# Kernel optimization log

Measured on AMD Instinct MI355X. Metric: run time of the kernel, lower is better.

## Reference

```python
import jax, jax.numpy as jnp
import numpy as np

STRIDES = (8.0, 16.0, 32.0)
ANCHORS = np.array([[[12,16],[19,36],[40,28]],
                    [[36,75],[76,55],[72,146]],
                    [[142,110],[192,243],[459,401]]], dtype=np.float32)  # [3 levels, 3 anchors, 2] in input pixels
INPUT_SIZE = 416.0
IGNORE_THRESHOLD = 0.5
EPS = 1e-7
MAX_BOXES = 64  # fixed cap on true boxes per image for jit-able ignore-mask
NC = 80


def _bce_logits(logits, targets):
    # numerically-stable binary cross entropy with logits, elementwise
    return jnp.maximum(logits, 0.0) - logits * targets + jnp.log1p(jnp.exp(-jnp.abs(logits)))


def _iou_xywh(b1, b2):
    # center-format boxes, broadcastable; returns IoU over last dim pair
    a1 = b1[..., 2] * b1[..., 3]
    a2 = b2[..., 2] * b2[..., 3]
    lt = jnp.maximum(b1[..., :2] - b1[..., 2:] * 0.5, b2[..., :2] - b2[..., 2:] * 0.5)
    rb = jnp.minimum(b1[..., :2] + b1[..., 2:] * 0.5, b2[..., :2] + b2[..., 2:] * 0.5)
    wh = jnp.maximum(rb - lt, 0.0)
    inter = wh[..., 0] * wh[..., 1]
    union = a1 + a2 - inter
    return inter / jnp.maximum(union, 1e-9)


def _level_loss(feature, label, idx):
    N, C, H, W = feature.shape
    f = feature.transpose(0, 2, 3, 1).reshape(N, H, W, 3, -1)
    raw_xy, raw_wh = f[..., 0:2], f[..., 2:4]
    raw_conf, raw_prob = f[..., 4:5], f[..., 5:]

    label_xywh = label[..., 0:4]
    label_conf = label[..., 4:5]
    label_prob = label[..., 5:]

    stride = STRIDES[idx]
    anchors = jnp.asarray(ANCHORS[idx])  # [3,2]

    gy, gx = jnp.meshgrid(jnp.arange(H, dtype=f.dtype), jnp.arange(W, dtype=f.dtype), indexing='ij')
    grid = jnp.stack([gx, gy], axis=-1)[:, :, None, :]  # [H,W,1,2]

    # decode predictions (GeneratePrediction)
    pred_xy = (jax.nn.sigmoid(raw_xy) + grid) * stride
    pred_wh = jnp.exp(raw_wh) * anchors
    pred_xywh = jnp.concatenate([pred_xy, pred_wh], axis=-1)  # [N,H,W,3,4]

    xy_offset = label_xywh[..., :2] / stride - grid
    wh_offset = label_conf * jnp.log(label_xywh[..., 2:4] / anchors + EPS)
    bbox_loss_scale = 2.0 - label_xywh[..., 2:3] * label_xywh[..., 3:4] / (INPUT_SIZE * INPUT_SIZE)

    # ignore mask: max IoU of each prediction against this image's true boxes
    conf_flat = label_conf[..., 0].reshape(N, -1)          # [N, H*W*3]
    boxes_flat = label_xywh.reshape(N, -1, 4)              # [N, H*W*3, 4]
    k = min(MAX_BOXES, conf_flat.shape[1])
    vals, idxs = jax.lax.top_k(conf_flat, k)               # positives first (conf is 0/1)
    true_boxes = jnp.take_along_axis(boxes_flat, idxs[..., None], axis=1)  # [N,k,4]
    valid = vals > 0.0                                     # [N,k]
    iou = _iou_xywh(pred_xywh[..., None, :], true_boxes[:, None, None, None, :, :])  # [N,H,W,3,k]
    iou = jnp.where(valid[:, None, None, None, :], iou, 0.0)
    max_iou = jnp.max(iou, axis=-1)                        # [N,H,W,3]; 0 when no valid boxes
    ignore_mask = (max_iou < IGNORE_THRESHOLD).astype(f.dtype)[..., None]

    xy_loss = label_conf * bbox_loss_scale * _bce_logits(raw_xy, xy_offset)
    wh_loss = label_conf * bbox_loss_scale * 0.5 * jnp.square(raw_wh - wh_offset)
    bce_conf = _bce_logits(raw_conf, label_conf)
    conf_loss = label_conf * bce_conf + (1.0 - label_conf) * ignore_mask * bce_conf
    prob_loss = label_conf * _bce_logits(raw_prob, label_prob)

    sum_axes = (1, 2, 3, 4)
    reg = jnp.mean(jnp.sum(xy_loss, axis=sum_axes)) + jnp.mean(jnp.sum(wh_loss, axis=sum_axes))
    conf = jnp.mean(jnp.sum(conf_loss, axis=sum_axes))
    prob = jnp.mean(jnp.sum(prob_loss, axis=sum_axes))
    return reg, conf, prob


def _make_label(key, N, H, W, p_pos):
    kc, kxy, kwh, kp = jax.random.split(key, 4)
    conf = (jax.random.uniform(kc, (N, H, W, 3, 1)) < p_pos).astype(jnp.float32)
    xy = jax.random.uniform(kxy, (N, H, W, 3, 2)) * INPUT_SIZE
    wh = jax.random.uniform(kwh, (N, H, W, 3, 2)) * 190.0 + 10.0  # strictly positive
    prob = (jax.random.uniform(kp, (N, H, W, 3, NC)) < 0.0125).astype(jnp.float32)
    return jnp.concatenate([xy, wh, conf, prob], axis=-1)


def setup_inputs() -> dict:
    key = jax.random.key(0)
    ks = jax.random.split(key, 6)
    N, C = 16, 3 * (5 + NC)
    sizes = [52, 26, 13]
    preds = [jax.random.normal(ks[i], (N, C, s, s), dtype=jnp.float32) for i, s in enumerate(sizes)]
    labels = [_make_label(ks[3 + i], N, s, s, 0.0008) for i, s in enumerate(sizes)]
    return {"pred0": preds[0], "pred1": preds[1], "pred2": preds[2],
            "label0": labels[0], "label1": labels[1], "label2": labels[2]}


def reference(pred0, pred1, pred2, label0, label1, label2):
    reg = conf = prob = 0.0
    for i, (f, l) in enumerate([(pred0, label0), (pred1, label1), (pred2, label2)]):
        r, c, p = _level_loss(f, l, i)
        reg, conf, prob = reg + r, conf + c, prob + p
    return (reg, conf, prob)
```

## Files before the change

kernel.cpp:

```cpp
#include <hip/hip_runtime.h>


#define NIMG 16
#define MAXB 64

#define C0 (16 * 3 * 52 * 52)
#define C1 (16 * 3 * 26 * 26)
#define C2 (16 * 3 * 13 * 13)
#define CTOT (C0 + C1 + C2)
#define NBLK ((CTOT + 255) / 256)

#define WS_COUNTS   0
#define WS_BOXES    256
#define WS_CELLIDS  49408
#define WS_PARTIAL  65536

__device__ __constant__ float d_anchors[3][3][2] = {
    {{12.f, 16.f}, {19.f, 36.f}, {40.f, 28.f}},
    {{36.f, 75.f}, {76.f, 55.f}, {72.f, 146.f}},
    {{142.f, 110.f}, {192.f, 243.f}, {459.f, 401.f}}};

__device__ __forceinline__ float bce_logits(float x, float t) {
    return fmaxf(x, 0.f) - x * t + log1pf(expf(-fabsf(x)));
}

__global__ void scan_labels(const float* __restrict__ l0,
                            const float* __restrict__ l1,
                            const float* __restrict__ l2,
                            int* __restrict__ counts,
                            float4* __restrict__ boxes,
                            int* __restrict__ cellids) {
    int rec = blockIdx.x * blockDim.x + threadIdx.x;
    if (rec >= CTOT) return;

    const float* lab;
    int level, cell, hw3;
    if (rec < C0)           { level = 0; cell = rec;           lab = l0; hw3 = 3 * 52 * 52; }
    else if (rec < C0 + C1) { level = 1; cell = rec - C0;      lab = l1; hw3 = 3 * 26 * 26; }
    else                    { level = 2; cell = rec - C0 - C1; lab = l2; hw3 = 3 * 13 * 13; }

    const float* lp = lab + (size_t)cell * 85;
    float c = lp[4];
    if (c > 0.f) {
        int n = cell / hw3;
        int p = atomicAdd(&counts[level * NIMG + n], 1);
        if (p < MAXB) {
            float4 b;
            b.x = lp[0]; b.y = lp[1]; b.z = lp[2]; b.w = lp[3];
            boxes[(level * NIMG + n) * MAXB + p] = b;
            cellids[(level * NIMG + n) * MAXB + p] = cell;
        }
    }
}

__global__ void loss_fused(const float* __restrict__ f0,
                           const float* __restrict__ f1,
                           const float* __restrict__ f2,
                           const float* __restrict__ l0,
                           const float* __restrict__ l1,
                           const float* __restrict__ l2,
                           const int* __restrict__ counts,
                           const float4* __restrict__ boxes,
                           const int* __restrict__ cellids,
                           float* __restrict__ partial) {
    int lane = threadIdx.x & 63;
    int wid = threadIdx.x >> 6;

    if (blockIdx.x < NBLK) {
        int gid = blockIdx.x * blockDim.x + threadIdx.x;
        float conf = 0.f;

        if (gid < CTOT) {
            const float* f;
            int level, cell, W, HW;
            float stride;
            if (gid < C0)           { level = 0; cell = gid;           f = f0; W = 52; HW = 52 * 52; stride = 8.f; }
            else if (gid < C0 + C1) { level = 1; cell = gid - C0;      f = f1; W = 26; HW = 26 * 26; stride = 16.f; }
            else                    { level = 2; cell = gid - C0 - C1; f = f2; W = 13; HW = 13 * 13; stride = 32.f; }

            int hw = cell % HW;
            int na = cell / HW;
            int a = na % 3;
            int n = na / 3;
            int w = hw % W;
            int h = hw / W;
            int cell_lab = (n * HW + hw) * 3 + a;

            const float* fp = f + (size_t)n * 255 * HW + (size_t)a * 85 * HW + hw;
            float rx = fp[0];
            float ry = fp[HW];
            float rw = fp[2 * HW];
            float rh = fp[3 * HW];
            float rc = fp[4 * HW];

            float aw = d_anchors[level][a][0];
            float ah = d_anchors[level][a][1];
            float px = (1.f / (1.f + expf(-rx)) + (float)w) * stride;
            float py = (1.f / (1.f + expf(-ry)) + (float)h) * stride;
            float pw = expf(rw) * aw;
            float ph = expf(rh) * ah;

            int m = counts[level * NIMG + n];
            if (m > MAXB) m = MAXB;
            int base = (level * NIMG + n) * MAXB;
            float parea = pw * ph;
            float pl = px - pw * 0.5f, pr = px + pw * 0.5f;
            float pt = py - ph * 0.5f, pb = py + ph * 0.5f;
            float maxiou = 0.f;
            bool ispos = false;
            for (int i = 0; i < m; ++i) {
                float4 b = boxes[base + i];
                if (cellids[base + i] == cell_lab) ispos = true;
                float tl = b.x - b.z * 0.5f, tr = b.x + b.z * 0.5f;
                float tt = b.y - b.w * 0.5f, tb = b.y + b.w * 0.5f;
                float iw = fmaxf(fminf(pr, tr) - fmaxf(pl, tl), 0.f);
                float ih = fmaxf(fminf(pb, tb) - fmaxf(pt, tt), 0.f);
                float inter = iw * ih;
                float uni = parea + b.z * b.w - inter;
                float iou = inter / fmaxf(uni, 1e-9f);
                maxiou = fmaxf(maxiou, iou);
            }
            if (ispos)              conf = bce_logits(rc, 1.f);
            else if (maxiou < 0.5f) conf = bce_logits(rc, 0.f);
        }

        for (int off = 32; off > 0; off >>= 1) conf += __shfl_down(conf, off);
        __shared__ float sc[4];
        if (lane == 0) sc[wid] = conf;
        __syncthreads();
        if (threadIdx.x == 0)
            partial[1 * 1024 + blockIdx.x] = sc[0] + sc[1] + sc[2] + sc[3];

    } else {
        int pb = blockIdx.x - NBLK;
        int level = pb / NIMG;
        int n = pb % NIMG;
        const float *f, *lab;
        int W, HW; float stride;
        if (level == 0)      { f = f0; lab = l0; W = 52; HW = 52 * 52; stride = 8.f; }
        else if (level == 1) { f = f1; lab = l1; W = 26; HW = 26 * 26; stride = 16.f; }
        else                 { f = f2; lab = l2; W = 13; HW = 13 * 13; stride = 32.f; }

        int m = counts[pb];
        if (m > MAXB) m = MAXB;
        int bbase = pb * MAXB;

        float reg_acc = 0.f, prob_acc = 0.f;
        for (int i = wid; i < m; i += 4) {
            int cell = cellids[bbase + i];
            float4 b = boxes[bbase + i];
            int a = cell % 3;
            int hw = (cell / 3) % HW;
            int w = hw % W;
            int h = hw / W;
            const float* fp = f + ((size_t)n * 255 + (size_t)a * 85) * HW + hw;
            const float* lp = lab + (size_t)cell * 85;

            int ch1 = (lane < 40) ? (5 + lane) : ((lane < 44) ? (lane - 40) : 0);
            float g1 = fp[(size_t)ch1 * HW];
            float g2 = fp[(size_t)((lane < 40) ? (45 + lane) : 0) * HW];
            float t1 = lp[(lane < 40) ? (5 + lane) : 0];
            float t2 = lp[(lane < 40) ? (45 + lane) : 0];

            float pp = (lane < 40) ? (bce_logits(g1, t1) + bce_logits(g2, t2)) : 0.f;
            for (int off = 32; off > 0; off >>= 1) pp += __shfl_down(pp, off);

            float rx = __shfl(g1, 40);
            float ry = __shfl(g1, 41);
            float rw = __shfl(g1, 42);
            float rh = __shfl(g1, 43);
            if (lane == 0) {
                prob_acc += pp;
                float aw = d_anchors[level][a][0];
                float ah = d_anchors[level][a][1];
                float ox = b.x / stride - (float)w;
                float oy = b.y / stride - (float)h;
                float ow = logf(b.z / aw + 1e-7f);
                float oh = logf(b.w / ah + 1e-7f);
                float scale = 2.f - b.z * b.w * (1.f / (416.f * 416.f));
                float dw = rw - ow, dh = rh - oh;
                reg_acc += scale * (bce_logits(rx, ox) + bce_logits(ry, oy))
                         + scale * 0.5f * (dw * dw + dh * dh);
            }
        }

        __shared__ float sp[2][4];
        if (lane == 0) { sp[0][wid] = reg_acc; sp[1][wid] = prob_acc; }
        __syncthreads();
        if (threadIdx.x == 0) {
            partial[0 * 1024 + pb] = sp[0][0] + sp[0][1] + sp[0][2] + sp[0][3];
            partial[2 * 1024 + pb] = sp[1][0] + sp[1][1] + sp[1][2] + sp[1][3];
        }
    }
}

__global__ void finalize(const float* __restrict__ partial,
                         float* __restrict__ out) {
    float a0 = 0.f, a1 = 0.f, a2 = 0.f;
    for (int i = threadIdx.x; i < NBLK; i += 256) {
        a1 += partial[1 * 1024 + i];
        if (i < 48) {
            a0 += partial[0 * 1024 + i];
            a2 += partial[2 * 1024 + i];
        }
    }
    for (int off = 32; off > 0; off >>= 1) {
        a0 += __shfl_down(a0, off);
        a1 += __shfl_down(a1, off);
        a2 += __shfl_down(a2, off);
    }
    __shared__ float s[3][4];
    int lane = threadIdx.x & 63;
    int wid = threadIdx.x >> 6;
    if (lane == 0) { s[0][wid] = a0; s[1][wid] = a1; s[2][wid] = a2; }
    __syncthreads();
    if (threadIdx.x == 0) {
        out[0] = (s[0][0] + s[0][1] + s[0][2] + s[0][3]) * (1.f / 16.f);
        out[1] = (s[1][0] + s[1][1] + s[1][2] + s[1][3]) * (1.f / 16.f);
        out[2] = (s[2][0] + s[2][1] + s[2][2] + s[2][3]) * (1.f / 16.f);
    }
}

extern "C" void kernel_launch(void* const* d_in, const int* in_sizes, int n_in,
                              void* d_out, int out_size, void* d_ws, size_t ws_size,
                              hipStream_t stream) {
    const float* f0 = (const float*)d_in[0];
    const float* f1 = (const float*)d_in[1];
    const float* f2 = (const float*)d_in[2];
    const float* l0 = (const float*)d_in[3];
    const float* l1 = (const float*)d_in[4];
    const float* l2 = (const float*)d_in[5];
    float* out = (float*)d_out;

    int*    counts  = (int*)((char*)d_ws + WS_COUNTS);
    float4* boxes   = (float4*)((char*)d_ws + WS_BOXES);
    int*    cellids = (int*)((char*)d_ws + WS_CELLIDS);
    float*  partial = (float*)((char*)d_ws + WS_PARTIAL);

    hipMemsetAsync(d_ws, 0, 256, stream);

    scan_labels<<<NBLK, 256, 0, stream>>>(l0, l1, l2, counts, boxes, cellids);
    loss_fused<<<NBLK + 48, 256, 0, stream>>>(f0, f1, f2, l0, l1, l2,
                                              counts, boxes, cellids, partial);
    finalize<<<1, 256, 0, stream>>>(partial, out);
}
```

Baseline: 134.3 us.

## Fuse scan, loss and finalize into one kernel with grid barrier

Merges the three launches into a single persistent kernel. A software grid barrier, built from an atomic counter and spin-sleep, separates the label scan from the loss phase. The prediction loads for the confidence path are issued before the barrier so they overlap the wait, and the last block to finish does the final reduction. This removes two kernel launches and their gaps, but it relies on all of the roughly 700 blocks being co-resident to avoid deadlock, and it adds spin contention on the barrier counter.

```diff
diff --git a/kernel.cpp b/kernel.cpp
--- a/kernel.cpp
+++ b/kernel.cpp
@@ -9,8 +9,10 @@
 #define C2 (16 * 3 * 13 * 13)
 #define CTOT (C0 + C1 + C2)
 #define NBLK ((CTOT + 255) / 256)
+#define NALL (NBLK + 48)
 
 #define WS_COUNTS   0
+#define WS_SYNC     192
 #define WS_BOXES    256
 #define WS_CELLIDS  49408
 #define WS_PARTIAL  65536
@@ -24,60 +26,77 @@
     return fmaxf(x, 0.f) - x * t + log1pf(expf(-fabsf(x)));
 }
 
-__global__ void scan_labels(const float* __restrict__ l0,
-                            const float* __restrict__ l1,
-                            const float* __restrict__ l2,
-                            int* __restrict__ counts,
-                            float4* __restrict__ boxes,
-                            int* __restrict__ cellids) {
-    int rec = blockIdx.x * blockDim.x + threadIdx.x;
-    if (rec >= CTOT) return;
-
-    const float* lab;
-    int level, cell, hw3;
-    if (rec < C0)           { level = 0; cell = rec;           lab = l0; hw3 = 3 * 52 * 52; }
-    else if (rec < C0 + C1) { level = 1; cell = rec - C0;      lab = l1; hw3 = 3 * 26 * 26; }
-    else                    { level = 2; cell = rec - C0 - C1; lab = l2; hw3 = 3 * 13 * 13; }
-
-    const float* lp = lab + (size_t)cell * 85;
-    float c = lp[4];
-    if (c > 0.f) {
-        int n = cell / hw3;
-        int p = atomicAdd(&counts[level * NIMG + n], 1);
-        if (p < MAXB) {
-            float4 b;
-            b.x = lp[0]; b.y = lp[1]; b.z = lp[2]; b.w = lp[3];
-            boxes[(level * NIMG + n) * MAXB + p] = b;
-            cellids[(level * NIMG + n) * MAXB + p] = cell;
-        }
-    }
-}
-
-__global__ void loss_fused(const float* __restrict__ f0,
-                           const float* __restrict__ f1,
-                           const float* __restrict__ f2,
-                           const float* __restrict__ l0,
-                           const float* __restrict__ l1,
-                           const float* __restrict__ l2,
-                           const int* __restrict__ counts,
-                           const float4* __restrict__ boxes,
-                           const int* __restrict__ cellids,
-                           float* __restrict__ partial) {
-    int lane = threadIdx.x & 63;
-    int wid = threadIdx.x >> 6;
-
-    if (blockIdx.x < NBLK) {
-        int gid = blockIdx.x * blockDim.x + threadIdx.x;
+__global__ __launch_bounds__(256) void yolo_all(
+        const float* __restrict__ f0,
+        const float* __restrict__ f1,
+        const float* __restrict__ f2,
+        const float* __restrict__ l0,
+        const float* __restrict__ l1,
+        const float* __restrict__ l2,
+        int* __restrict__ counts,
+        int* __restrict__ sync,
+        float4* __restrict__ boxes,
+        int* __restrict__ cellids,
+        float* __restrict__ partial,
+        float* __restrict__ out) {
+    const int lane = threadIdx.x & 63;
+    const int wid  = threadIdx.x >> 6;
+    const int tid  = blockIdx.x * blockDim.x + threadIdx.x;
+
+    if (tid < CTOT) {
+        const float* lab;
+        int level, cell, hw3;
+        if (tid < C0)           { level = 0; cell = tid;           lab = l0; hw3 = 3 * 52 * 52; }
+        else if (tid < C0 + C1) { level = 1; cell = tid - C0;      lab = l1; hw3 = 3 * 26 * 26; }
+        else                    { level = 2; cell = tid - C0 - C1; lab = l2; hw3 = 3 * 13 * 13; }
+        const float* lp = lab + (size_t)cell * 85;
+        float c = lp[4];
+        if (c > 0.f) {
+            int n = cell / hw3;
+            int p = atomicAdd(&counts[level * NIMG + n], 1);
+            if (p < MAXB) {
+                float4 b;
+                b.x = lp[0]; b.y = lp[1]; b.z = lp[2]; b.w = lp[3];
+                boxes[(level * NIMG + n) * MAXB + p] = b;
+                cellids[(level * NIMG + n) * MAXB + p] = cell;
+            }
+        }
+    }
+
+    const bool is_conf = (blockIdx.x < NBLK);
+    float rx = 0.f, ry = 0.f, rw = 0.f, rh = 0.f, rc = 0.f;
+    int level = 0, cell = 0, W = 52, HW = 52 * 52;
+    float stride = 8.f;
+    const float* fcur = f0;
+    if (is_conf && tid < CTOT) {
+        if (tid < C0)           { level = 0; cell = tid;           fcur = f0; W = 52; HW = 52 * 52; stride = 8.f; }
+        else if (tid < C0 + C1) { level = 1; cell = tid - C0;      fcur = f1; W = 26; HW = 26 * 26; stride = 16.f; }
+        else                    { level = 2; cell = tid - C0 - C1; fcur = f2; W = 13; HW = 13 * 13; stride = 32.f; }
+        int hw = cell % HW;
+        int na = cell / HW;
+        int a = na % 3;
+        int n = na / 3;
+        const float* fp = fcur + (size_t)n * 255 * HW + (size_t)a * 85 * HW + hw;
+        rx = fp[0];
+        ry = fp[HW];
+        rw = fp[2 * HW];
+        rh = fp[3 * HW];
+        rc = fp[4 * HW];
+    }
+
+    __syncthreads();
+    if (threadIdx.x == 0) {
+        __threadfence();
+        atomicAdd(&sync[0], 1);
+        while (atomicAdd(&sync[0], 0) < NALL)
+            __builtin_amdgcn_s_sleep(2);
+        __threadfence();
+    }
+    __syncthreads();
+
+    if (is_conf) {
         float conf = 0.f;
-
-        if (gid < CTOT) {
-            const float* f;
-            int level, cell, W, HW;
-            float stride;
-            if (gid < C0)           { level = 0; cell = gid;           f = f0; W = 52; HW = 52 * 52; stride = 8.f; }
-            else if (gid < C0 + C1) { level = 1; cell = gid - C0;      f = f1; W = 26; HW = 26 * 26; stride = 16.f; }
-            else                    { level = 2; cell = gid - C0 - C1; f = f2; W = 13; HW = 13 * 13; stride = 32.f; }
-
+        if (tid < CTOT) {
             int hw = cell % HW;
             int na = cell / HW;
             int a = na % 3;
@@ -85,13 +104,6 @@
             int w = hw % W;
             int h = hw / W;
             int cell_lab = (n * HW + hw) * 3 + a;
-
-            const float* fp = f + (size_t)n * 255 * HW + (size_t)a * 85 * HW + hw;
-            float rx = fp[0];
-            float ry = fp[HW];
-            float rw = fp[2 * HW];
-            float rh = fp[3 * HW];
-            float rc = fp[4 * HW];
 
             float aw = d_anchors[level][a][0];
             float ah = d_anchors[level][a][1];
@@ -123,23 +135,21 @@
             if (ispos)              conf = bce_logits(rc, 1.f);
             else if (maxiou < 0.5f) conf = bce_logits(rc, 0.f);
         }
-
         for (int off = 32; off > 0; off >>= 1) conf += __shfl_down(conf, off);
         __shared__ float sc[4];
         if (lane == 0) sc[wid] = conf;
         __syncthreads();
         if (threadIdx.x == 0)
             partial[1 * 1024 + blockIdx.x] = sc[0] + sc[1] + sc[2] + sc[3];
-
     } else {
         int pb = blockIdx.x - NBLK;
-        int level = pb / NIMG;
+        int lv = pb / NIMG;
         int n = pb % NIMG;
         const float *f, *lab;
-        int W, HW; float stride;
-        if (level == 0)      { f = f0; lab = l0; W = 52; HW = 52 * 52; stride = 8.f; }
-        else if (level == 1) { f = f1; lab = l1; W = 26; HW = 26 * 26; stride = 16.f; }
-        else                 { f = f2; lab = l2; W = 13; HW = 13 * 13; stride = 32.f; }
+        int Wp, HWp; float strp;
+        if (lv == 0)      { f = f0; lab = l0; Wp = 52; HWp = 52 * 52; strp = 8.f; }
+        else if (lv == 1) { f = f1; lab = l1; Wp = 26; HWp = 26 * 26; strp = 16.f; }
+        else              { f = f2; lab = l2; Wp = 13; HWp = 13 * 13; strp = 32.f; }
 
         int m = counts[pb];
         if (m > MAXB) m = MAXB;
@@ -147,43 +157,42 @@
 
         float reg_acc = 0.f, prob_acc = 0.f;
         for (int i = wid; i < m; i += 4) {
-            int cell = cellids[bbase + i];
+            int pcell = cellids[bbase + i];
             float4 b = boxes[bbase + i];
-            int a = cell % 3;
-            int hw = (cell / 3) % HW;
-            int w = hw % W;
-            int h = hw / W;
-            const float* fp = f + ((size_t)n * 255 + (size_t)a * 85) * HW + hw;
-            const float* lp = lab + (size_t)cell * 85;
+            int a = pcell % 3;
+            int hw = (pcell / 3) % HWp;
+            int w = hw % Wp;
+            int h = hw / Wp;
+            const float* fp = f + ((size_t)n * 255 + (size_t)a * 85) * HWp + hw;
+            const float* lp = lab + (size_t)pcell * 85;
 
             int ch1 = (lane < 40) ? (5 + lane) : ((lane < 44) ? (lane - 40) : 0);
-            float g1 = fp[(size_t)ch1 * HW];
-            float g2 = fp[(size_t)((lane < 40) ? (45 + lane) : 0) * HW];
+            float g1 = fp[(size_t)ch1 * HWp];
+            float g2 = fp[(size_t)((lane < 40) ? (45 + lane) : 0) * HWp];
             float t1 = lp[(lane < 40) ? (5 + lane) : 0];
             float t2 = lp[(lane < 40) ? (45 + lane) : 0];
 
             float pp = (lane < 40) ? (bce_logits(g1, t1) + bce_logits(g2, t2)) : 0.f;
             for (int off = 32; off > 0; off >>= 1) pp += __shfl_down(pp, off);
 
-            float rx = __shfl(g1, 40);
-            float ry = __shfl(g1, 41);
-            float rw = __shfl(g1, 42);
-            float rh = __shfl(g1, 43);
+            float prx = __shfl(g1, 40);
+            float pry = __shfl(g1, 41);
+            float prw = __shfl(g1, 42);
+            float prh = __shfl(g1, 43);
             if (lane == 0) {
                 prob_acc += pp;
-                float aw = d_anchors[level][a][0];
-                float ah = d_anchors[level][a][1];
-                float ox = b.x / stride - (float)w;
-                float oy = b.y / stride - (float)h;
+                float aw = d_anchors[lv][a][0];
+                float ah = d_anchors[lv][a][1];
+                float ox = b.x / strp - (float)w;
+                float oy = b.y / strp - (float)h;
                 float ow = logf(b.z / aw + 1e-7f);
                 float oh = logf(b.w / ah + 1e-7f);
                 float scale = 2.f - b.z * b.w * (1.f / (416.f * 416.f));
-                float dw = rw - ow, dh = rh - oh;
-                reg_acc += scale * (bce_logits(rx, ox) + bce_logits(ry, oy))
+                float dw = prw - ow, dh = prh - oh;
+                reg_acc += scale * (bce_logits(prx, ox) + bce_logits(pry, oy))
                          + scale * 0.5f * (dw * dw + dh * dh);
             }
         }
-
         __shared__ float sp[2][4];
         if (lane == 0) { sp[0][wid] = reg_acc; sp[1][wid] = prob_acc; }
         __syncthreads();
@@ -192,32 +201,38 @@
             partial[2 * 1024 + pb] = sp[1][0] + sp[1][1] + sp[1][2] + sp[1][3];
         }
     }
-}
-
-__global__ void finalize(const float* __restrict__ partial,
-                         float* __restrict__ out) {
-    float a0 = 0.f, a1 = 0.f, a2 = 0.f;
-    for (int i = threadIdx.x; i < NBLK; i += 256) {
-        a1 += partial[1 * 1024 + i];
-        if (i < 48) {
-            a0 += partial[0 * 1024 + i];
-            a2 += partial[2 * 1024 + i];
-        }
-    }
-    for (int off = 32; off > 0; off >>= 1) {
-        a0 += __shfl_down(a0, off);
-        a1 += __shfl_down(a1, off);
-        a2 += __shfl_down(a2, off);
-    }
-    __shared__ float s[3][4];
-    int lane = threadIdx.x & 63;
-    int wid = threadIdx.x >> 6;
-    if (lane == 0) { s[0][wid] = a0; s[1][wid] = a1; s[2][wid] = a2; }
+
+    __shared__ int amlast;
     __syncthreads();
     if (threadIdx.x == 0) {
-        out[0] = (s[0][0] + s[0][1] + s[0][2] + s[0][3]) * (1.f / 16.f);
-        out[1] = (s[1][0] + s[1][1] + s[1][2] + s[1][3]) * (1.f / 16.f);
-        out[2] = (s[2][0] + s[2][1] + s[2][2] + s[2][3]) * (1.f / 16.f);
+        __threadfence();
+        int d = atomicAdd(&sync[1], 1);
+        amlast = (d == NALL - 1) ? 1 : 0;
+    }
+    __syncthreads();
+    if (amlast) {
+        __threadfence();
+        float a0 = 0.f, a1 = 0.f, a2 = 0.f;
+        for (int i = threadIdx.x; i < NBLK; i += 256) {
+            a1 += partial[1 * 1024 + i];
+            if (i < 48) {
+                a0 += partial[0 * 1024 + i];
+                a2 += partial[2 * 1024 + i];
+            }
+        }
+        for (int off = 32; off > 0; off >>= 1) {
+            a0 += __shfl_down(a0, off);
+            a1 += __shfl_down(a1, off);
+            a2 += __shfl_down(a2, off);
+        }
+        __shared__ float s[3][4];
+        if (lane == 0) { s[0][wid] = a0; s[1][wid] = a1; s[2][wid] = a2; }
+        __syncthreads();
+        if (threadIdx.x == 0) {
+            out[0] = (s[0][0] + s[0][1] + s[0][2] + s[0][3]) * (1.f / 16.f);
+            out[1] = (s[1][0] + s[1][1] + s[1][2] + s[1][3]) * (1.f / 16.f);
+            out[2] = (s[2][0] + s[2][1] + s[2][2] + s[2][3]) * (1.f / 16.f);
+        }
     }
 }
 
@@ -233,14 +248,14 @@
     float* out = (float*)d_out;
 
     int*    counts  = (int*)((char*)d_ws + WS_COUNTS);
+    int*    syncp   = (int*)((char*)d_ws + WS_SYNC);
     float4* boxes   = (float4*)((char*)d_ws + WS_BOXES);
     int*    cellids = (int*)((char*)d_ws + WS_CELLIDS);
     float*  partial = (float*)((char*)d_ws + WS_PARTIAL);
 
     hipMemsetAsync(d_ws, 0, 256, stream);
 
-    scan_labels<<<NBLK, 256, 0, stream>>>(l0, l1, l2, counts, boxes, cellids);
-    loss_fused<<<NBLK + 48, 256, 0, stream>>>(f0, f1, f2, l0, l1, l2,
-                                              counts, boxes, cellids, partial);
-    finalize<<<1, 256, 0, stream>>>(partial, out);
+    yolo_all<<<NALL, 256, 0, stream>>>(f0, f1, f2, l0, l1, l2,
+                                       counts, syncp, boxes, cellids,
+                                       partial, out);
 }
```

After: 225.0 us. +67.5%, slower.
